# Kernel tuning notes

Hardware: AMD Instinct MI355X
Metric: run time of the kernel (lower is better)

The kernel has to match this reference:

```python
import jax, jax.numpy as jnp
import numpy as np

HEADS = 8
DIM_HEAD = 64
SCALE = DIM_HEAD ** (-0.5)


def setup_inputs() -> dict:
    key = jax.random.key(0)
    k1, k2, k3 = jax.random.split(key, 3)
    b, l, c = 8, 4096, 512
    x = jax.random.normal(k1, (b, l, c), dtype=jnp.float32)
    w_qkv = jax.random.normal(k2, (3 * c, c), dtype=jnp.float32) * (c ** -0.5)
    w_out = jax.random.normal(k3, (c, c), dtype=jnp.float32) * (c ** -0.5)
    b_out = jnp.zeros((c,), dtype=jnp.float32)
    return {"x": x, "w_qkv": w_qkv, "w_out": w_out, "b_out": b_out}


def reference(x, w_qkv, w_out, b_out):
    b, l, c = x.shape
    h = HEADS
    lh = l // h
    # to_qkv: Linear(dim, 3*dim, bias=False)
    qkv = x @ w_qkv.T                                   # (b, l, 3c)
    qkv = qkv.reshape(b, lh, h, 3, c).transpose(3, 0, 2, 1, 4)  # (3, b, h, l/h, c)
    q, k, v = qkv[0], qkv[1], qkv[2]                    # each (b, h, l/h, c)
    # transpose(-2,-1): attention is over the CHANNEL axis
    q = jnp.swapaxes(q, -2, -1)                         # (b, h, c, l/h)
    k = jnp.swapaxes(k, -2, -1)                         # (b, h, c, l/h)
    v = jnp.swapaxes(v, -2, -1)                         # (b, h, c, l/h)
    attn = jnp.einsum('bhcl,bhdl->bhcd', q, k) * SCALE  # (b, h, c, c)
    attn = jax.nn.softmax(attn, axis=-1)
    y = jnp.einsum('bhcd,bhdl->bhcl', attn, v)          # (b, h, c, l/h)
    y = y.transpose(0, 3, 1, 2).reshape(b, l, c)        # (b, l/h, h, c) -> (b, l, c)
    # to_out: Linear(dim, dim) + Dropout (identity at eval)
    out = y @ w_out.T + b_out
    return out
```

## Files before the change

kernel.cpp:

```cpp
#include <hip/hip_runtime.h>
#include <stdint.h>
#include <stddef.h>

typedef _Float16 f16;
typedef _Float16 f16x8 __attribute__((ext_vector_type(8)));
typedef _Float16 f16x4 __attribute__((ext_vector_type(4)));
typedef float f32x4 __attribute__((ext_vector_type(4)));

__device__ __forceinline__ void gload16(const void* g, void* l) {
    auto gp = (const __attribute__((address_space(1))) uint32_t*)(uintptr_t)g;
    auto lp = (__attribute__((address_space(3))) uint32_t*)(uintptr_t)l;
    __builtin_amdgcn_global_load_lds(gp, lp, 16, 0, 0);
}

__device__ __forceinline__ f16x4 cvt4(f32x4 v) {
    return f16x4{ (f16)v[0], (f16)v[1], (f16)v[2], (f16)v[3] };
}

__global__ __launch_bounds__(256) void prep_k(const float* __restrict__ x,
                                              const float* __restrict__ wqkv,
                                              const float* __restrict__ wout,
                                              f16* __restrict__ xb,
                                              f16* __restrict__ wqb,
                                              f16* __restrict__ wob) {
    int tid = blockIdx.x * blockDim.x + threadIdx.x;
    int stride = gridDim.x * blockDim.x;
    for (int i = tid; i < 4194304; i += stride) {
        float4 v = ((const float4*)x)[i];
        *(f16x4*)(xb + (size_t)i * 4) = f16x4{ (f16)v.x, (f16)v.y, (f16)v.z, (f16)v.w };
    }
    for (int i = tid; i < 196608; i += stride) {
        float4 v = ((const float4*)wqkv)[i];
        *(f16x4*)(wqb + (size_t)i * 4) = f16x4{ (f16)v.x, (f16)v.y, (f16)v.z, (f16)v.w };
    }
    for (int i = tid; i < 65536; i += stride) {
        float4 v = ((const float4*)wout)[i];
        *(f16x4*)(wob + (size_t)i * 4) = f16x4{ (f16)v.x, (f16)v.y, (f16)v.z, (f16)v.w };
    }
}

#define W0  asm volatile("s_waitcnt vmcnt(0)" ::: "memory")
#define BAR __builtin_amdgcn_s_barrier()

#define A_STAGE(NB) do {                                                        \
    gload16(Ab + kb + sE,          &ldsA[NB][( 0 + wid*8)*64]);                 \
    gload16(Ab + kb + sO + 32768,  &ldsA[NB][(32 + wid*8)*64]);                 \
    gload16(Ab + kb + sE + 65536,  &ldsA[NB][(64 + wid*8)*64]);                 \
    gload16(Ab + kb + sO + 98304,  &ldsA[NB][(96 + wid*8)*64]);                 \
    gload16(Bb + kb + sE,          &ldsB[NB][( 0 + wid*8)*64]);                 \
    gload16(Bb + kb + sO + 32768,  &ldsB[NB][(32 + wid*8)*64]);                 \
    gload16(Bb + kb + sE + 65536,  &ldsB[NB][(64 + wid*8)*64]);                 \
    gload16(Bb + kb + sO + 98304,  &ldsB[NB][(96 + wid*8)*64]);                 \
    kb += 128;                                                                  \
} while (0)

#define A_RD(SET, BUF) do {                                                     \
    _Pragma("unroll") for (int mi = 0; mi < 4; ++mi)                            \
    _Pragma("unroll") for (int kk = 0; kk < 2; ++kk)                            \
        aF##SET[mi][kk] = *(const f16x8*)(&ldsA[BUF][0] + aoff[mi][kk]);        \
    _Pragma("unroll") for (int ni = 0; ni < 4; ++ni)                            \
    _Pragma("unroll") for (int kk = 0; kk < 2; ++kk)                            \
        bF##SET[ni][kk] = *(const f16x8*)(&ldsB[BUF][0] + boff[ni][kk]);        \
} while (0)

#define A_MM(SET, KK, ML, MH_) do {                                             \
    __builtin_amdgcn_s_setprio(1);                                              \
    if (qk) {                                                                   \
        _Pragma("unroll") for (int mi = ML; mi < MH_; ++mi)                     \
        _Pragma("unroll") for (int ni = 0; ni < 4; ++ni)                        \
            acc[mi][ni] = __builtin_amdgcn_mfma_f32_16x16x32_f16(               \
                aF##SET[mi][KK], bF##SET[ni][KK], acc[mi][ni], 0, 0, 0);        \
    } else {                                                                    \
        _Pragma("unroll") for (int mi = ML; mi < MH_; ++mi)                     \
        _Pragma("unroll") for (int ni = 0; ni < 4; ++ni)                        \
            acc[mi][ni] = __builtin_amdgcn_mfma_f32_16x16x32_f16(               \
                bF##SET[ni][KK], aF##SET[mi][KK], acc[mi][ni], 0, 0, 0);        \
    }                                                                           \
    __builtin_amdgcn_s_setprio(0);                                              \
} while (0)

#define A_MM3(SET)   do { A_MM(SET, 0, 0, 2); A_MM(SET, 0, 2, 4); A_MM(SET, 1, 0, 2); } while (0)
#define A_MMLAST(SET) A_MM(SET, 1, 2, 4)

#define A_TILE(CUR, NXT, NB, STG, FINAL) do {                                   \
    if (STG) A_STAGE(NB);                                                       \
    A_MM3(CUR);                                                                 \
    if (!FINAL) { W0; BAR; A_RD(NXT, NB); }                                     \
    A_MMLAST(CUR);                                                              \
} while (0)

__global__ __launch_bounds__(256, 2) void g15_k(const f16* __restrict__ A0,
                                                const f16* __restrict__ B0,
                                                f16* __restrict__ Qd,
                                                f16* __restrict__ Kd,
                                                f16* __restrict__ Vd) {
    __shared__ f16 ldsA[2][8192];
    __shared__ f16 ldsB[2][8192];

    const int tid = threadIdx.x;
    const int lane = tid & 63;
    const int wid = tid >> 6;
    const int wr = wid >> 1;
    const int wc = wid & 1;

    const int bid = blockIdx.x;
    const bool qk = bid < 2048;
    int tm, tn;
    if (qk) {
        int swz = (bid & 7) * 256 + (bid >> 3);
        tm = (swz >> 3) * 128; tn = (swz & 7) * 128;
    } else {
        int b2 = bid - 2048;
        int swz = (b2 & 7) * 128 + (b2 >> 3);
        tm = (swz >> 2) * 128; tn = (swz & 3) * 128 + 1024;
    }

    const char* Ab = (const char*)(A0 + (size_t)tm * 512);
    const char* Bb = (const char*)(B0 + (size_t)tn * 512);

    const int u = tid >> 3;
    const int colE = ((tid & 7) ^ ((u & 7) ^ (u >> 3))) * 16;
    const int sE = u * 1024 + colE;
    const int sO = sE ^ 64;
    int kb = 0;

    int aoff[4][2], boff[4][2];
#pragma unroll
    for (int mi = 0; mi < 4; ++mi) {
        int r = qk ? ((lane & 15) * 8 + wr * 4 + mi)
                   : (wr * 64 + mi * 16 + (lane & 15));
#pragma unroll
        for (int kk = 0; kk < 2; ++kk) {
            int c8 = (lane >> 4) + kk * 4;
            aoff[mi][kk] = r * 64 + (c8 ^ ((r & 7) ^ ((r >> 3) & 7))) * 8;
        }
    }
#pragma unroll
    for (int ni = 0; ni < 4; ++ni) {
        int r = wc * 64 + ni * 16 + (lane & 15);
#pragma unroll
        for (int kk = 0; kk < 2; ++kk) {
            int c8 = (lane >> 4) + kk * 4;
            boff[ni][kk] = r * 64 + (c8 ^ ((r & 7) ^ ((r >> 3) & 7))) * 8;
        }
    }

    f32x4 acc[4][4] = {};
    f16x8 aF0[4][2], bF0[4][2], aF1[4][2], bF1[4][2];

    A_STAGE(0);
    W0; BAR;
    A_RD(0, 0);

#pragma unroll 1
    for (int i = 0; i < 3; ++i) {
        A_TILE(0, 1, 1, true, false);
        A_TILE(1, 0, 0, true, false);
    }
    A_TILE(0, 1, 1, true, false);
    A_TILE(1, 1, 1, false, true);

    if (qk) {
        const int b = tm >> 12;
        const int lt = (tm & 4095) >> 3;
        f16* dst = (tn < 512) ? Qd : Kd;
        const int cb = (tn & 511) + wc * 64;
        const int lh0 = lt + (lane >> 4) * 4;
#pragma unroll
        for (int mi = 0; mi < 4; ++mi) {
            int h = wr * 4 + mi;
#pragma unroll
            for (int ni = 0; ni < 4; ++ni) {
                int c = cb + ni * 16 + (lane & 15);
                *(f16x4*)(dst + ((size_t)((b * 8 + h) * 512 + c)) * 512 + lh0) =
                    cvt4(acc[mi][ni]);
            }
        }
    } else {
        f16* dst = Vd;
#pragma unroll
        for (int mi = 0; mi < 4; ++mi) {
            int t = tm + wr * 64 + mi * 16 + (lane & 15);
            int b = t >> 12, l = t & 4095;
            int h = l & 7, lh = l >> 3;
#pragma unroll
            for (int ni = 0; ni < 4; ++ni) {
                int d0 = (tn - 1024) + wc * 64 + ni * 16 + (lane >> 4) * 4;
                *(f16x4*)(dst + ((size_t)((b * 8 + h) * 512 + lh)) * 512 + d0) =
                    cvt4(acc[mi][ni]);
            }
        }
    }
}


#define F_STAGE(B) do {                                                         \
    gload16(Qt + kb + soff,           &L[65536 + (B)*8192 + ( 0 + wid*8)*64]);  \
    gload16(Qt + kb + soff + 65536,   &L[65536 + (B)*8192 + (64 + wid*8)*64]);  \
    gload16(Kt + kb + soff,           &L[(B)*32768 + (  0 + wid*8)*64]);        \
    gload16(Kt + kb + soff + 65536,   &L[(B)*32768 + ( 64 + wid*8)*64]);        \
    gload16(Kt + kb + soff + 131072,  &L[(B)*32768 + (128 + wid*8)*64]);        \
    gload16(Kt + kb + soff + 196608,  &L[(B)*32768 + (192 + wid*8)*64]);        \
    gload16(Kt + kb + soff + 262144,  &L[(B)*32768 + (256 + wid*8)*64]);        \
    gload16(Kt + kb + soff + 327680,  &L[(B)*32768 + (320 + wid*8)*64]);        \
    gload16(Kt + kb + soff + 393216,  &L[(B)*32768 + (384 + wid*8)*64]);        \
    gload16(Kt + kb + soff + 458752,  &L[(B)*32768 + (448 + wid*8)*64]);        \
    kb += 128;                                                                  \
} while (0)

#define F_RD(KK, B) do {                                                        \
    _Pragma("unroll") for (int ni = 0; ni < 4; ++ni)                            \
        bF[ni] = *(const f16x8*)(&L[(B)*32768] + boff[ni][KK]);                 \
    _Pragma("unroll") for (int mi = 0; mi < 8; ++mi)                            \
        aF[mi] = *(const f16x8*)(&L[65536 + (B)*8192] + aoff[mi][KK]);          \
} while (0)

#define F_MM do {                                                               \
    __builtin_amdgcn_s_setprio(1);                                              \
    _Pragma("unroll") for (int mi = 0; mi < 8; ++mi)                            \
    _Pragma("unroll") for (int ni = 0; ni < 4; ++ni)                            \
        acc[mi][ni] = __builtin_amdgcn_mfma_f32_16x16x32_f16(                   \
            aF[mi], bF[ni], acc[mi][ni], 0, 0, 0);                              \
    __builtin_amdgcn_s_setprio(0);                                              \
} while (0)

__global__ __launch_bounds__(512) void attn_k(const f16* __restrict__ Qb,
                                              const f16* __restrict__ Kb,
                                              const f16* __restrict__ Vb,
                                              f16* __restrict__ yb) {
    __shared__ __align__(16) f16 L[81920];

    const int tid = threadIdx.x;
    const int lane = tid & 63;
    const int wid = tid >> 6;
    const int g = lane >> 4;
    const int li = lane & 15;

    const int bid = blockIdx.x;
    const int swz = (bid & 7) * 32 + (bid >> 3);
    const int bh = swz >> 2, ct = swz & 3;
    const int b = bh >> 3, h = bh & 7;

    const char* Qt = (const char*)(Qb + (size_t)bh * 262144 + (size_t)ct * 128 * 512);
    const char* Kt = (const char*)(Kb + (size_t)bh * 262144);
    const char* Vt = (const char*)(Vb + (size_t)bh * 262144);

    const int soff = (tid >> 3) * 1024 +
                     ((((lane & 7) ^ (lane >> 3) ^ wid) & 7) * 16);
    int kb = 0;

    int aoff[8][2], boff[4][2];
#pragma unroll
    for (int mi = 0; mi < 8; ++mi) {
        int r = mi * 16 + li;
        int s3 = (r & 7) ^ ((r >> 3) & 7);
#pragma unroll
        for (int kk = 0; kk < 2; ++kk)
            aoff[mi][kk] = r * 64 + (((g + kk * 4) ^ s3)) * 8;
    }
#pragma unroll
    for (int ni = 0; ni < 4; ++ni) {
        int r = wid * 64 + ni * 16 + li;
        int s3 = (r & 7) ^ ((r >> 3) & 7);
#pragma unroll
        for (int kk = 0; kk < 2; ++kk)
            boff[ni][kk] = r * 64 + (((g + kk * 4) ^ s3)) * 8;
    }

    f32x4 acc[8][4] = {};
    f16x8 aF[8], bF[4];

    F_STAGE(0);
#pragma unroll 1
    for (int t = 0; t < 8; ++t) {
        const int cb = t & 1;
        if (t < 7) {
            F_STAGE(cb ^ 1);
            asm volatile("s_waitcnt vmcnt(10)" ::: "memory");
        } else {
            W0;
        }
        BAR;
        F_RD(0, cb);
        F_MM;
        F_RD(1, cb);
        F_MM;
        BAR;
    }

    const int voff = (lane >> 2) * 1024 +
                     ((((lane & 3) ^ ((lane >> 2) & 3) ^ g) & 3) * 16);
    f16x8 vr[4];
#pragma unroll
    for (int i = 0; i < 4; ++i)
        vr[i] = *(const f16x8*)(Vt + (size_t)((wid * 4 + i) * 16) * 1024 + voff);

    float* red  = (float*)&L[65536];
    float* redg = (float*)&L[65536 + 2048];

#pragma unroll
    for (int mi = 0; mi < 8; ++mi)
#pragma unroll
        for (int ni = 0; ni < 4; ++ni) acc[mi][ni] *= 0.125f;

#pragma unroll
    for (int mi = 0; mi < 8; ++mi)
#pragma unroll
        for (int j = 0; j < 4; ++j) {
            float v = fmaxf(fmaxf(acc[mi][0][j], acc[mi][1][j]),
                            fmaxf(acc[mi][2][j], acc[mi][3][j]));
#pragma unroll
            for (int off = 1; off < 16; off <<= 1) v = fmaxf(v, __shfl_xor(v, off, 64));
            if (li == 0) red[wid * 128 + mi * 16 + g * 4 + j] = v;
        }
    BAR;
    if (tid < 128) {
        float m = red[tid];
#pragma unroll
        for (int w = 1; w < 8; ++w) m = fmaxf(m, red[w * 128 + tid]);
        redg[tid] = m;
    }
    BAR;

#pragma unroll
    for (int mi = 0; mi < 8; ++mi)
#pragma unroll
        for (int j = 0; j < 4; ++j) {
            float mg = redg[mi * 16 + g * 4 + j];
            float s = 0.f;
#pragma unroll
            for (int ni = 0; ni < 4; ++ni) {
                float e = __expf(acc[mi][ni][j] - mg);
                acc[mi][ni][j] = e;
                s += e;
            }
#pragma unroll
            for (int off = 1; off < 16; off <<= 1) s += __shfl_xor(s, off, 64);
            if (li == 0) red[wid * 128 + mi * 16 + g * 4 + j] = s;
        }
    BAR;
    if (tid < 128) {
        float s = red[tid];
#pragma unroll
        for (int w = 1; w < 8; ++w) s += red[w * 128 + tid];
        redg[tid] = 1.0f / s;
    }
    BAR;

#pragma unroll
    for (int mi = 0; mi < 8; ++mi)
#pragma unroll
        for (int j = 0; j < 4; ++j) {
            int c = mi * 16 + g * 4 + j;
            int s3c = (c & 7) ^ ((c >> 3) & 7);
            float is = redg[c];
#pragma unroll
            for (int ni = 0; ni < 4; ++ni) {
                int dch = wid * 8 + ni * 2 + (li >> 3);
                L[c * 512 + ((dch ^ s3c) << 3) + (li & 7)] =
                    (f16)(acc[mi][ni][j] * is);
            }
        }
    BAR;

#pragma unroll
    for (int mi = 0; mi < 8; ++mi)
#pragma unroll
        for (int ni = 0; ni < 4; ++ni) acc[mi][ni] = f32x4{0.f, 0.f, 0.f, 0.f};

#pragma unroll 1
    for (int dt = 0; dt < 16; ++dt) {
#pragma unroll
        for (int i = 0; i < 4; ++i)
            *(f16x8*)&L[65536 + (wid * 4 + i) * 512 + lane * 8] = vr[i];
        if (dt < 15) {
#pragma unroll
            for (int i = 0; i < 4; ++i)
                vr[i] = *(const f16x8*)(Vt + (size_t)((wid * 4 + i) * 16) * 1024 +
                                        (dt + 1) * 64 + voff);
        }
        asm volatile("s_waitcnt lgkmcnt(0)" ::: "memory");
        BAR;
        f16x8 aP[8], bV[4];
#pragma unroll
        for (int mi = 0; mi < 8; ++mi) {
            int c = mi * 16 + li;
            int s3c = (c & 7) ^ ((c >> 3) & 7);
            aP[mi] = *(const f16x8*)&L[c * 512 + (((dt * 4 + g) ^ s3c) << 3)];
        }
#pragma unroll
        for (int ni = 0; ni < 4; ++ni) {
            int lr = wid * 64 + ni * 16 + li;
            int s2 = (lr & 3) ^ ((lr >> 2) & 3);
            bV[ni] = *(const f16x8*)&L[65536 + lr * 32 + ((g ^ s2) & 3) * 8];
        }
        __builtin_amdgcn_s_setprio(1);
#pragma unroll
        for (int mi = 0; mi < 8; ++mi)
#pragma unroll
            for (int ni = 0; ni < 4; ++ni)
                acc[mi][ni] = __builtin_amdgcn_mfma_f32_16x16x32_f16(
                    aP[mi], bV[ni], acc[mi][ni], 0, 0, 0);
        __builtin_amdgcn_s_setprio(0);
        BAR;
    }

#pragma unroll
    for (int mi = 0; mi < 8; ++mi) {
        int c0 = ct * 128 + mi * 16 + g * 4;
#pragma unroll
        for (int ni = 0; ni < 4; ++ni) {
            int l = wid * 64 + ni * 16 + li;
            size_t tok = (size_t)b * 4096 + (size_t)l * 8 + h;
            *(f16x4*)(yb + tok * 512 + c0) = cvt4(acc[mi][ni]);
        }
    }
}

#define B_STAGE(NB) do {                                                        \
    gload16(At + soff,          &ldsA2[NB][(  0 + wid*8)*64]);                  \
    gload16(At + soff + 65536,  &ldsA2[NB][( 64 + wid*8)*64]);                  \
    gload16(At + soff + 131072, &ldsA2[NB][(128 + wid*8)*64]);                  \
    gload16(At + soff + 196608, &ldsA2[NB][(192 + wid*8)*64]);                  \
    gload16(Bt + soff,          &ldsB2[NB][(  0 + wid*8)*64]);                  \
    gload16(Bt + soff + 65536,  &ldsB2[NB][( 64 + wid*8)*64]);                  \
    gload16(Bt + soff + 131072, &ldsB2[NB][(128 + wid*8)*64]);                  \
    gload16(Bt + soff + 196608, &ldsB2[NB][(192 + wid*8)*64]);                  \
    At += 128; Bt += 128;                                                       \
} while (0)

#define B_RD12(KK, BUF) do {                                                    \
    _Pragma("unroll") for (int ni = 0; ni < 4; ++ni)                            \
        bF[ni] = *(const f16x8*)(&ldsB2[BUF][0] + boff[ni][KK]);                \
    _Pragma("unroll") for (int mi = 0; mi < 8; ++mi)                            \
        aF[mi] = *(const f16x8*)(&ldsA2[BUF][0] + aoff[mi][KK]);                \
} while (0)

#define B_MM32 do {                                                             \
    __builtin_amdgcn_s_setprio(1);                                              \
    _Pragma("unroll") for (int mi = 0; mi < 8; ++mi)                            \
    _Pragma("unroll") for (int ni = 0; ni < 4; ++ni)                            \
        acc[mi][ni] = __builtin_amdgcn_mfma_f32_16x16x32_f16(                   \
            bF[ni], aF[mi], acc[mi][ni], 0, 0, 0);                              \
    __builtin_amdgcn_s_setprio(0);                                              \
} while (0)

#define B_TILE(CB, NB, STG, FINAL) do {                                         \
    B_RD12(0, CB);                                                              \
    if (STG) B_STAGE(NB);                                                       \
    B_MM32;                                                                     \
    B_RD12(1, CB);                                                              \
    B_MM32;                                                                     \
    if (!FINAL) { W0; BAR; }                                                    \
} while (0)

__global__ __launch_bounds__(512) void out_k(const f16* __restrict__ A0,
                                             const f16* __restrict__ B0,
                                             float* __restrict__ O,
                                             const float* __restrict__ bias) {
    __shared__ f16 ldsA2[2][16384];
    __shared__ f16 ldsB2[2][16384];

    const int tid = threadIdx.x;
    const int lane = tid & 63;
    const int wid = tid >> 6;
    const int wr = wid >> 2;
    const int wc = wid & 3;

    const int bid = blockIdx.x;
    int swz = (bid & 7) * 32 + (bid >> 3);
    int tm = (swz >> 1) * 256, tn = (swz & 1) * 256;

    const char* At = (const char*)(A0 + (size_t)tm * 512);
    const char* Bt = (const char*)(B0 + (size_t)tn * 512);

    const int soff = wid * 8192 + (lane >> 3) * 1024 +
                     ((((lane & 7) ^ (lane >> 3) ^ wid) & 7) * 16);

    int aoff[8][2], boff[4][2];
#pragma unroll
    for (int mi = 0; mi < 8; ++mi) {
        int r = wr * 128 + mi * 16 + (lane & 15);
        int s3 = (r & 7) ^ ((r >> 3) & 7);
#pragma unroll
        for (int kk = 0; kk < 2; ++kk)
            aoff[mi][kk] = r * 64 + ((((lane >> 4) + kk * 4) ^ s3)) * 8;
    }
#pragma unroll
    for (int ni = 0; ni < 4; ++ni) {
        int r = wc * 64 + ni * 16 + (lane & 15);
        int s3 = (r & 7) ^ ((r >> 3) & 7);
#pragma unroll
        for (int kk = 0; kk < 2; ++kk)
            boff[ni][kk] = r * 64 + ((((lane >> 4) + kk * 4) ^ s3)) * 8;
    }

    f32x4 acc[8][4] = {};
    f16x8 aF[8], bF[4];

    B_STAGE(0);
    W0; BAR;

#pragma unroll 1
    for (int i = 0; i < 3; ++i) {
        B_TILE(0, 1, true, false);
        B_TILE(1, 0, true, false);
    }
    B_TILE(0, 1, true, false);
    B_TILE(1, 1, false, true);

#pragma unroll
    for (int mi = 0; mi < 8; ++mi) {
        int m = tm + wr * 128 + mi * 16 + (lane & 15);
#pragma unroll
        for (int ni = 0; ni < 4; ++ni) {
            int n0 = tn + wc * 64 + ni * 16 + (lane >> 4) * 4;
            float4 bv = *(const float4*)(bias + n0);
            f32x4 v = acc[mi][ni];
            v[0] += bv.x; v[1] += bv.y; v[2] += bv.z; v[3] += bv.w;
            *(f32x4*)(O + (size_t)m * 512 + n0) = v;
        }
    }
}

extern "C" void kernel_launch(void* const* d_in, const int* in_sizes, int n_in,
                              void* d_out, int out_size, void* d_ws, size_t ws_size,
                              hipStream_t stream) {
    const float* x = (const float*)d_in[0];
    const float* wqkv = (const float*)d_in[1];
    const float* wout = (const float*)d_in[2];
    const float* bout = (const float*)d_in[3];
    float* out = (float*)d_out;
    char* ws = (char*)d_ws;
    const size_t MBs = 1u << 20;

    f16* xb  = (f16*)(ws + 0);
    f16* wqb = (f16*)(ws + 32 * MBs);
    f16* wob = (f16*)(ws + 34 * MBs);
    f16* Qb  = (f16*)(ws + 35 * MBs);
    f16* Kb  = (f16*)(ws + 67 * MBs);
    f16* Vb  = (f16*)(ws + 99 * MBs);
    f16* yb  = xb;

    prep_k<<<1024, 256, 0, stream>>>(x, wqkv, wout, xb, wqb, wob);
    g15_k<<<3072, 256, 0, stream>>>(xb, wqb, Qb, Kb, Vb);
    attn_k<<<256, 512, 0, stream>>>(Qb, Kb, Vb, yb);
    out_k<<<256, 512, 0, stream>>>(yb, wob, out, bout);
}
```

Before: 185.2 us.

## Fuse fp32-to-fp16 conversion of x into the QKV GEMM load path

Removes the separate pass that converts x to fp16. The QKV GEMM now reads fp32 x straight into registers, converts it, and writes swizzled fp16 into LDS. Weights still use async global-to-LDS loads. This saves a 64MB read plus a 32MB write and re-read of x, but the GEMM now reads twice the bytes for A through registers instead of async LDS loads. That costs extra VGPRs and an lgkmcnt wait before the barrier, which may hurt load/compute overlap.

Result: slower. 273.6 us (+47.7%).

```diff
diff --git a/kernel.cpp b/kernel.cpp
--- a/kernel.cpp
+++ b/kernel.cpp
@@ -17,18 +17,12 @@
     return f16x4{ (f16)v[0], (f16)v[1], (f16)v[2], (f16)v[3] };
 }
 
-__global__ __launch_bounds__(256) void prep_k(const float* __restrict__ x,
-                                              const float* __restrict__ wqkv,
+__global__ __launch_bounds__(256) void prep_k(const float* __restrict__ wqkv,
                                               const float* __restrict__ wout,
-                                              f16* __restrict__ xb,
                                               f16* __restrict__ wqb,
                                               f16* __restrict__ wob) {
     int tid = blockIdx.x * blockDim.x + threadIdx.x;
     int stride = gridDim.x * blockDim.x;
-    for (int i = tid; i < 4194304; i += stride) {
-        float4 v = ((const float4*)x)[i];
-        *(f16x4*)(xb + (size_t)i * 4) = f16x4{ (f16)v.x, (f16)v.y, (f16)v.z, (f16)v.w };
-    }
     for (int i = tid; i < 196608; i += stride) {
         float4 v = ((const float4*)wqkv)[i];
         *(f16x4*)(wqb + (size_t)i * 4) = f16x4{ (f16)v.x, (f16)v.y, (f16)v.z, (f16)v.w };
@@ -42,11 +36,31 @@
 #define W0  asm volatile("s_waitcnt vmcnt(0)" ::: "memory")
 #define BAR __builtin_amdgcn_s_barrier()
 
-#define A_STAGE(NB) do {                                                        \
-    gload16(Ab + kb + sE,          &ldsA[NB][( 0 + wid*8)*64]);                 \
-    gload16(Ab + kb + sO + 32768,  &ldsA[NB][(32 + wid*8)*64]);                 \
-    gload16(Ab + kb + sE + 65536,  &ldsA[NB][(64 + wid*8)*64]);                 \
-    gload16(Ab + kb + sO + 98304,  &ldsA[NB][(96 + wid*8)*64]);                 \
+
+#define LOADX do {                                                              \
+    xr[0] = *(const float4*)(Xb + kb2 + sEX);                                   \
+    xr[1] = *(const float4*)(Xb + kb2 + sEX + 16);                              \
+    xr[2] = *(const float4*)(Xb + kb2 + sOX + 65536);                           \
+    xr[3] = *(const float4*)(Xb + kb2 + sOX + 65536 + 16);                      \
+    xr[4] = *(const float4*)(Xb + kb2 + sEX + 131072);                          \
+    xr[5] = *(const float4*)(Xb + kb2 + sEX + 131072 + 16);                     \
+    xr[6] = *(const float4*)(Xb + kb2 + sOX + 196608);                          \
+    xr[7] = *(const float4*)(Xb + kb2 + sOX + 196608 + 16);                     \
+    kb2 += 256;                                                                 \
+} while (0)
+
+#define CVTW(NB) do {                                                           \
+    _Pragma("unroll") for (int c = 0; c < 4; ++c) {                             \
+        f16x8 v;                                                                \
+        v[0] = (f16)xr[c*2].x; v[1] = (f16)xr[c*2].y;                           \
+        v[2] = (f16)xr[c*2].z; v[3] = (f16)xr[c*2].w;                           \
+        v[4] = (f16)xr[c*2+1].x; v[5] = (f16)xr[c*2+1].y;                       \
+        v[6] = (f16)xr[c*2+1].z; v[7] = (f16)xr[c*2+1].w;                       \
+        *(f16x8*)&ldsA[NB][(c * 32 + wid * 8) * 64 + lane * 8] = v;             \
+    }                                                                           \
+} while (0)
+
+#define BSTG(NB) do {                                                           \
     gload16(Bb + kb + sE,          &ldsB[NB][( 0 + wid*8)*64]);                 \
     gload16(Bb + kb + sO + 32768,  &ldsB[NB][(32 + wid*8)*64]);                 \
     gload16(Bb + kb + sE + 65536,  &ldsB[NB][(64 + wid*8)*64]);                 \
@@ -83,13 +97,19 @@
 #define A_MMLAST(SET) A_MM(SET, 1, 2, 4)
 
 #define A_TILE(CUR, NXT, NB, STG, FINAL) do {                                   \
-    if (STG) A_STAGE(NB);                                                       \
+    if (STG) { LOADX; BSTG(NB); }                                               \
     A_MM3(CUR);                                                                 \
-    if (!FINAL) { W0; BAR; A_RD(NXT, NB); }                                     \
+    if (!FINAL) {                                                               \
+        CVTW(NB);                                                               \
+        W0;                                                                     \
+        asm volatile("s_waitcnt lgkmcnt(0)" ::: "memory");                      \
+        BAR;                                                                    \
+        A_RD(NXT, NB);                                                          \
+    }                                                                           \
     A_MMLAST(CUR);                                                              \
 } while (0)
 
-__global__ __launch_bounds__(256, 2) void g15_k(const f16* __restrict__ A0,
+__global__ __launch_bounds__(256, 2) void g16_k(const float* __restrict__ X0,
                                                 const f16* __restrict__ B0,
                                                 f16* __restrict__ Qd,
                                                 f16* __restrict__ Kd,
@@ -115,14 +135,17 @@
         tm = (swz >> 2) * 128; tn = (swz & 3) * 128 + 1024;
     }
 
-    const char* Ab = (const char*)(A0 + (size_t)tm * 512);
+    const char* Xb = (const char*)(X0 + (size_t)tm * 512);
     const char* Bb = (const char*)(B0 + (size_t)tn * 512);
 
     const int u = tid >> 3;
     const int colE = ((tid & 7) ^ ((u & 7) ^ (u >> 3))) * 16;
     const int sE = u * 1024 + colE;
     const int sO = sE ^ 64;
-    int kb = 0;
+    const int sEX = u * 2048 + colE * 2;
+    const int sOX = sEX ^ 128;
+    int kb = 0, kb2 = 0;
+    float4 xr[8];
 
     int aoff[4][2], boff[4][2];
 #pragma unroll
@@ -148,8 +171,12 @@
     f32x4 acc[4][4] = {};
     f16x8 aF0[4][2], bF0[4][2], aF1[4][2], bF1[4][2];
 
-    A_STAGE(0);
-    W0; BAR;
+    LOADX;
+    BSTG(0);
+    CVTW(0);
+    W0;
+    asm volatile("s_waitcnt lgkmcnt(0)" ::: "memory");
+    BAR;
     A_RD(0, 0);
 
 #pragma unroll 1
@@ -192,7 +219,6 @@
         }
     }
 }
-
 
 #define F_STAGE(B) do {                                                         \
     gload16(Qt + kb + soff,           &L[65536 + (B)*8192 + ( 0 + wid*8)*64]);  \
@@ -534,16 +560,15 @@
     char* ws = (char*)d_ws;
     const size_t MBs = 1u << 20;
 
-    f16* xb  = (f16*)(ws + 0);
+    f16* yb  = (f16*)(ws + 0);
     f16* wqb = (f16*)(ws + 32 * MBs);
     f16* wob = (f16*)(ws + 34 * MBs);
     f16* Qb  = (f16*)(ws + 35 * MBs);
     f16* Kb  = (f16*)(ws + 67 * MBs);
     f16* Vb  = (f16*)(ws + 99 * MBs);
-    f16* yb  = xb;
-
-    prep_k<<<1024, 256, 0, stream>>>(x, wqkv, wout, xb, wqb, wob);
-    g15_k<<<3072, 256, 0, stream>>>(xb, wqb, Qb, Kb, Vb);
+
+    prep_k<<<256, 256, 0, stream>>>(wqkv, wout, wqb, wob);
+    g16_k<<<3072, 256, 0, stream>>>(x, wqb, Qb, Kb, Vb);
     attn_k<<<256, 512, 0, stream>>>(Qb, Kb, Vb, yb);
     out_k<<<256, 512, 0, stream>>>(yb, wob, out, bout);
 }
```
